# Performance work log

Hardware: AMD Instinct MI355X
Metric: run time of the kernel (lower is better)

## Reference

```python
import jax, jax.numpy as jnp
import numpy as np

HEADS = 8

def setup_inputs() -> dict:
    key = jax.random.key(0)
    k1, k2, k3 = jax.random.split(key, 3)
    B, C, L = 8, 512, 4096
    dim_head = 64
    hidden = HEADS * dim_head  # 512
    x = jax.random.normal(k1, (B, C, L), dtype=jnp.float32)
    # Conv1d(dim, hidden*3, 1, bias=False) -> weight [hidden*3, dim]
    w_qkv = jax.random.normal(k2, (hidden * 3, C), dtype=jnp.float32) * 0.02
    # Conv1d(hidden, dim, 1) -> weight [dim, hidden], bias [dim]
    w_out = jax.random.normal(k3, (C, hidden), dtype=jnp.float32) * 0.02
    b_out = jnp.zeros((C,), dtype=jnp.float32)
    return {"x": x, "w_qkv": w_qkv, "w_out": w_out, "b_out": b_out}

def reference(x, w_qkv, w_out, b_out):
    B, C, L = x.shape
    # 1x1 Conv1d == channel matmul
    qkv = jnp.einsum('oc,bcl->bol', w_qkv, x)            # [B, 3*H*dh, L]
    qkv = qkv.reshape(B, 3, HEADS, -1, L)                # qkv outermost, then heads, then c
    q, k, v = qkv[:, 0], qkv[:, 1], qkv[:, 2]            # each [B, H, dh, L]
    k = jax.nn.softmax(k, axis=-1)                       # softmax over sequence
    context = jnp.einsum('bhdn,bhen->bhde', k, v)        # [B, H, dh, dh]
    out = jnp.einsum('bhde,bhdn->bhen', context, q)      # [B, H, dh, L]
    out = out.reshape(B, -1, L)                          # [B, H*dh, L]
    return jnp.einsum('oc,bcl->bol', w_out, out) + b_out[None, :, None]
```

## Files before the change

### kernel.cpp

```cpp
#include <hip/hip_runtime.h>
#include <hip/hip_bf16.h>


typedef __bf16 bf16x8 __attribute__((ext_vector_type(8)));
typedef __bf16 bf16x4 __attribute__((ext_vector_type(4)));
typedef float  f32x4  __attribute__((ext_vector_type(4)));

#define B_  8
#define L_  4096
#define C_  512

#define GLD_LDS16(g, l)                                             \
    __builtin_amdgcn_global_load_lds(                               \
        (const __attribute__((address_space(1))) void*)(g),         \
        (__attribute__((address_space(3))) void*)(l), 16, 0, 0)

#define FENCE asm volatile("" ::: "memory")
#define BAR   do { FENCE; __builtin_amdgcn_s_barrier(); FENCE; } while (0)
#define DRAIN_LGKM asm volatile("s_waitcnt lgkmcnt(0)" ::: "memory")
#define WAIT_VM(N) asm volatile("s_waitcnt vmcnt(" #N ")" ::: "memory")

__global__ __launch_bounds__(256) void prep_all(const float* __restrict__ x,
                                                __hip_bfloat16* __restrict__ xt,
                                                const float* __restrict__ wqkv_f,
                                                __hip_bfloat16* __restrict__ wkv_b,
                                                __hip_bfloat16* __restrict__ wqT,
                                                float* __restrict__ zero_base) {
    __shared__ float tile[64 * 132];
    int blk = blockIdx.x;
    int t = threadIdx.x;
    if (blk < 2048) {
        int b = blk >> 8, rem = blk & 255;
        int l0 = (rem & 31) * 128, c0 = (rem >> 5) * 64;
        const float* xp = x + ((size_t)b * C_ + c0) * L_ + l0;
#pragma unroll
        for (int p = 0; p < 8; p++) {
            int i = p * 8 + (t >> 5);
            int j = (t & 31) * 4;
            float4 vv = *(const float4*)(xp + (size_t)i * L_ + j);
            *(float4*)&tile[i * 132 + j] = vv;
        }
        __syncthreads();
        unsigned short* xo = (unsigned short*)xt + ((size_t)b * L_ + l0) * C_ + c0;
#pragma unroll
        for (int qq = 0; qq < 8; qq++) {
            int l = qq * 16 + (t >> 4);
            int cg = (t & 15) * 4;
            bf16x4 ov;
#pragma unroll
            for (int k = 0; k < 4; k++) ov[k] = (__bf16)tile[(cg + k) * 132 + l];
            *(bf16x4*)(xo + (size_t)l * C_ + cg) = ov;
        }
    } else if (blk < 4096) {
        int i = (blk - 2048) * 256 + t;
        wkv_b[i] = __float2bfloat16(wqkv_f[512 * 512 + i]);
    } else if (blk < 4352) {
        int tb = blk - 4096;
        int r0 = (tb >> 4) * 32, c0 = (tb & 15) * 32;
        int tx = t & 31, ty = t >> 5;
        for (int r = 0; r < 32; r += 8)
            tile[(ty + r) * 33 + tx] = wqkv_f[(size_t)(r0 + ty + r) * 512 + c0 + tx];
        __syncthreads();
        for (int r = 0; r < 32; r += 8)
            wqT[(size_t)(c0 + ty + r) * 512 + r0 + tx] = __float2bfloat16(tile[tx * 33 + ty + r]);
    } else {
        int i = (blk - 4352) * 256 + t;
        zero_base[i] = 0.f;
    }
}

__global__ __launch_bounds__(256, 2) void gemm_kv(
    const __hip_bfloat16* __restrict__ A, const __hip_bfloat16* __restrict__ Bt,
    float* __restrict__ ctx, float* __restrict__ Ssum) {
    __shared__ alignas(16) unsigned short sA[2][128 * 64];
    __shared__ alignas(16) unsigned short sB[2][128 * 64];

    const int K = C_;
    int b = blockIdx.z, h = blockIdx.y;
    int n0 = blockIdx.x * 128;
    const __hip_bfloat16* Bb = Bt + (size_t)b * L_ * C_;

    int t = threadIdx.x;
    int lane = t & 63, wv = t >> 6;
    int l16 = lane & 15, q4 = lane >> 4;
    int wr = (wv >> 1) * 64, wc = (wv & 1) * 64;

    int srow = lane >> 3;
    int swz  = ((lane & 7) ^ srow) * 8;

    const __hip_bfloat16* gA[4];
    const __hip_bfloat16* gB[4];
    unsigned ldoff[4];
#pragma unroll
    for (int c = 0; c < 4; c++) {
        int r = c * 32 + wv * 8;
        int lr = r + srow;
        int grow = h * 64 + lr + (lr >= 64 ? 448 : 0);
        gA[c] = A + (size_t)grow * K + swz;
        gB[c] = Bb + (size_t)(n0 + lr) * K + swz;
        ldoff[c] = (unsigned)r * 64;
    }

    int gsel0 = (q4 ^ (l16 & 7)) * 8;
    int gsel1 = gsel0 ^ 32;
    unsigned rA = (unsigned)(wr + l16) * 64;
    unsigned rB = (unsigned)(wc + l16) * 64;
    const int NKT = K >> 6;

    f32x4 acc[4][4] = {};
    bf16x8 aF[4][2], bF[4][2];

#pragma unroll
    for (int c = 0; c < 4; c++) GLD_LDS16(gA[c], &sA[0][ldoff[c]]);
#pragma unroll
    for (int c = 0; c < 4; c++) GLD_LDS16(gB[c], &sB[0][ldoff[c]]);
#pragma unroll
    for (int c = 0; c < 4; c++) GLD_LDS16(gA[c] + 64, &sA[1][ldoff[c]]);
    WAIT_VM(4);
    BAR;

#pragma unroll 1
    for (int kt = 0; kt < NKT; ++kt) {
        int cur = kt & 1, nbuf = cur ^ 1;
        const unsigned short* As_b = sA[cur];
        const unsigned short* Bs_b = sB[cur];
        bool st1 = (kt + 1) < NKT;
        bool st2 = (kt + 2) < NKT;

#pragma unroll
        for (int i = 0; i < 4; i++) {
            aF[i][0] = *(const bf16x8*)&As_b[rA + i * 1024 + gsel0];
            aF[i][1] = *(const bf16x8*)&As_b[rA + i * 1024 + gsel1];
        }
#pragma unroll
        for (int j = 0; j < 2; j++) {
            bF[j][0] = *(const bf16x8*)&Bs_b[rB + j * 1024 + gsel0];
            bF[j][1] = *(const bf16x8*)&Bs_b[rB + j * 1024 + gsel1];
        }
        if (st1) {
            int ko = (kt + 1) << 6;
#pragma unroll
            for (int c = 0; c < 4; c++) GLD_LDS16(gB[c] + ko, &sB[nbuf][ldoff[c]]);
        }
        BAR;
        __builtin_amdgcn_s_setprio(1);
#pragma unroll
        for (int ks = 0; ks < 2; ks++)
#pragma unroll
            for (int i = 0; i < 4; i++)
#pragma unroll
                for (int j = 0; j < 2; j++)
                    acc[i][j] = __builtin_amdgcn_mfma_f32_16x16x32_bf16(aF[i][ks], bF[j][ks], acc[i][j], 0, 0, 0);
        __builtin_amdgcn_s_setprio(0);
        DRAIN_LGKM;
        BAR;

#pragma unroll
        for (int j = 2; j < 4; j++) {
            bF[j][0] = *(const bf16x8*)&Bs_b[rB + j * 1024 + gsel0];
            bF[j][1] = *(const bf16x8*)&Bs_b[rB + j * 1024 + gsel1];
        }
        if (st2) {
            int ko = (kt + 2) << 6;
#pragma unroll
            for (int c = 0; c < 4; c++) GLD_LDS16(gA[c] + ko, &sA[cur][ldoff[c]]);
        }
        BAR;
        __builtin_amdgcn_s_setprio(1);
#pragma unroll
        for (int ks = 0; ks < 2; ks++)
#pragma unroll
            for (int i = 0; i < 4; i++)
#pragma unroll
                for (int j = 0; j < 2; j++)
                    acc[i][2 + j] = __builtin_amdgcn_mfma_f32_16x16x32_bf16(aF[i][ks], bF[2 + j][ks], acc[i][2 + j], 0, 0, 0);
        __builtin_amdgcn_s_setprio(0);
        DRAIN_LGKM;
        if (st2) { WAIT_VM(4); } else { WAIT_VM(0); }
        BAR;
    }

    __bf16* Pb = (__bf16*)sA;
    __bf16* Vb = (__bf16*)sB;
    float* ctxg = ctx  + ((size_t)b * 8 + h) * 4096;
    float* Sg   = Ssum + ((size_t)b * 8 + h) * 64;

    if (wv < 2) {
#pragma unroll
        for (int i = 0; i < 4; i++)
#pragma unroll
            for (int r = 0; r < 4; r++) {
                int d = i * 16 + q4 * 4 + r;
                float rs = 0.f;
#pragma unroll
                for (int j = 0; j < 4; j++) {
                    int n = wc + j * 16 + l16;
                    float pv = __expf(acc[i][j][r]);
                    rs += pv;
                    Pb[d * 128 + (((n >> 3) ^ (d & 15)) * 8) + (n & 7)] = (__bf16)pv;
                }
                rs += __shfl_xor(rs, 1, 64);
                rs += __shfl_xor(rs, 2, 64);
                rs += __shfl_xor(rs, 4, 64);
                rs += __shfl_xor(rs, 8, 64);
                if (l16 == 0) atomicAdd(&Sg[d], rs);
            }
    } else {
#pragma unroll
        for (int i = 0; i < 4; i++)
#pragma unroll
            for (int j = 0; j < 4; j++)
#pragma unroll
                for (int r = 0; r < 4; r++) {
                    int e = i * 16 + q4 * 4 + r;
                    int n = wc + j * 16 + l16;
                    Vb[e * 128 + (((n >> 3) ^ (e & 15)) * 8) + (n & 7)] = (__bf16)acc[i][j][r];
                }
    }
    DRAIN_LGKM;
    BAR;

    f32x4 acc2[4] = {};
#pragma unroll
    for (int kk = 0; kk < 4; kk++) {
        int gg = kk * 4 + q4;
        bf16x8 bf2 = *(const bf16x8*)&Vb[(wv * 16 + l16) * 128 + ((gg ^ l16) * 8)];
#pragma unroll
        for (int i2 = 0; i2 < 4; i2++) {
            bf16x8 af2 = *(const bf16x8*)&Pb[(i2 * 16 + l16) * 128 + ((gg ^ l16) * 8)];
            acc2[i2] = __builtin_amdgcn_mfma_f32_16x16x32_bf16(af2, bf2, acc2[i2], 0, 0, 0);
        }
    }
#pragma unroll
    for (int i2 = 0; i2 < 4; i2++)
#pragma unroll
        for (int r = 0; r < 4; r++) {
            int d = i2 * 16 + q4 * 4 + r;
            int e = wv * 16 + l16;
            atomicAdd(&ctxg[d * 64 + e], acc2[i2][r]);
        }
}

__global__ __launch_bounds__(256, 2) void gemm_p(
    const __hip_bfloat16* __restrict__ A, const __hip_bfloat16* __restrict__ Bt,
    size_t strideA, size_t strideB, int M, int N, int K,
    float* __restrict__ outb, const float* __restrict__ bias) {
    __shared__ alignas(16) unsigned short sA[2][128 * 64];
    __shared__ alignas(16) unsigned short sB[2][128 * 64];

    int b = blockIdx.z;
    int m0 = blockIdx.y * 128, n0 = blockIdx.x * 128;
    const __hip_bfloat16* Ab = A + strideA * (size_t)b;
    const __hip_bfloat16* Bb = Bt + strideB * (size_t)b;

    int t = threadIdx.x;
    int lane = t & 63, wv = t >> 6;
    int l16 = lane & 15, q4 = lane >> 4;
    int wr = (wv >> 1) * 64, wc = (wv & 1) * 64;

    int srow = lane >> 3;
    int swz  = ((lane & 7) ^ srow) * 8;

    const __hip_bfloat16* gA[4];
    const __hip_bfloat16* gB[4];
    unsigned ldoff[4];
#pragma unroll
    for (int c = 0; c < 4; c++) {
        int r = c * 32 + wv * 8;
        gA[c] = Ab + (size_t)(m0 + r + srow) * K + swz;
        gB[c] = Bb + (size_t)(n0 + r + srow) * K + swz;
        ldoff[c] = (unsigned)r * 64;
    }

    int gsel0 = (q4 ^ (l16 & 7)) * 8;
    int gsel1 = gsel0 ^ 32;
    unsigned rA = (unsigned)(wr + l16) * 64;
    unsigned rB = (unsigned)(wc + l16) * 64;
    int NKT = K >> 6;

    f32x4 acc[4][4] = {};
    bf16x8 aF[4][2], bF[4][2];

#pragma unroll
    for (int c = 0; c < 4; c++) GLD_LDS16(gA[c], &sA[0][ldoff[c]]);
#pragma unroll
    for (int c = 0; c < 4; c++) GLD_LDS16(gB[c], &sB[0][ldoff[c]]);
    if (NKT > 1) {
#pragma unroll
        for (int c = 0; c < 4; c++) GLD_LDS16(gA[c] + 64, &sA[1][ldoff[c]]);
        WAIT_VM(4);
    } else {
        WAIT_VM(0);
    }
    BAR;

#pragma unroll 1
    for (int kt = 0; kt < NKT; ++kt) {
        int cur = kt & 1, nbuf = cur ^ 1;
        const unsigned short* As_b = sA[cur];
        const unsigned short* Bs_b = sB[cur];
        bool st1 = (kt + 1) < NKT;
        bool st2 = (kt + 2) < NKT;

#pragma unroll
        for (int i = 0; i < 4; i++) {
            aF[i][0] = *(const bf16x8*)&As_b[rA + i * 1024 + gsel0];
            aF[i][1] = *(const bf16x8*)&As_b[rA + i * 1024 + gsel1];
        }
#pragma unroll
        for (int j = 0; j < 2; j++) {
            bF[j][0] = *(const bf16x8*)&Bs_b[rB + j * 1024 + gsel0];
            bF[j][1] = *(const bf16x8*)&Bs_b[rB + j * 1024 + gsel1];
        }
        if (st1) {
            int ko = (kt + 1) << 6;
#pragma unroll
            for (int c = 0; c < 4; c++) GLD_LDS16(gB[c] + ko, &sB[nbuf][ldoff[c]]);
        }
        BAR;
        __builtin_amdgcn_s_setprio(1);
#pragma unroll
        for (int ks = 0; ks < 2; ks++)
#pragma unroll
            for (int i = 0; i < 4; i++)
#pragma unroll
                for (int j = 0; j < 2; j++)
                    acc[i][j] = __builtin_amdgcn_mfma_f32_16x16x32_bf16(aF[i][ks], bF[j][ks], acc[i][j], 0, 0, 0);
        __builtin_amdgcn_s_setprio(0);
        DRAIN_LGKM;
        BAR;

#pragma unroll
        for (int j = 2; j < 4; j++) {
            bF[j][0] = *(const bf16x8*)&Bs_b[rB + j * 1024 + gsel0];
            bF[j][1] = *(const bf16x8*)&Bs_b[rB + j * 1024 + gsel1];
        }
        if (st2) {
            int ko = (kt + 2) << 6;
#pragma unroll
            for (int c = 0; c < 4; c++) GLD_LDS16(gA[c] + ko, &sA[cur][ldoff[c]]);
        }
        BAR;
        __builtin_amdgcn_s_setprio(1);
#pragma unroll
        for (int ks = 0; ks < 2; ks++)
#pragma unroll
            for (int i = 0; i < 4; i++)
#pragma unroll
                for (int j = 0; j < 2; j++)
                    acc[i][2 + j] = __builtin_amdgcn_mfma_f32_16x16x32_bf16(aF[i][ks], bF[2 + j][ks], acc[i][2 + j], 0, 0, 0);
        __builtin_amdgcn_s_setprio(0);
        DRAIN_LGKM;
        if (st2) { WAIT_VM(4); } else { WAIT_VM(0); }
        BAR;
    }

#pragma unroll
    for (int i = 0; i < 4; i++)
#pragma unroll
        for (int j = 0; j < 4; j++)
#pragma unroll
            for (int r = 0; r < 4; r++) {
                int row = m0 + wr + i * 16 + q4 * 4 + r;
                int col = n0 + wc + j * 16 + l16;
                outb[((size_t)b * M + row) * (size_t)N + col] = acc[i][j][r] + bias[row];
            }
}

__global__ __launch_bounds__(256) void gemm_bt(
    const __hip_bfloat16* __restrict__ A, const __hip_bfloat16* __restrict__ Bt,
    size_t strideA, size_t strideB, int M, int N, int K,
    __hip_bfloat16* __restrict__ obf) {
    __shared__ alignas(16) unsigned short As[128 * 64];
    __shared__ alignas(16) unsigned short Bs[128 * 64];

    int b = blockIdx.z;
    int m0 = blockIdx.y * 128, n0 = blockIdx.x * 128;
    const __hip_bfloat16* Ab = A + strideA * (size_t)b;
    const __hip_bfloat16* Bb = Bt + strideB * (size_t)b;

    int t = threadIdx.x;
    int lane = t & 63, wv = t >> 6;
    int l16 = lane & 15, q4 = lane >> 4;
    int wr = (wv >> 1) * 64, wc = (wv & 1) * 64;

    int srow = lane >> 3;
    int swz  = ((lane & 7) ^ srow) * 8;

    const __hip_bfloat16* gA[4];
    const __hip_bfloat16* gB[4];
    unsigned short* lA[4];
    unsigned short* lB[4];
#pragma unroll
    for (int c = 0; c < 4; c++) {
        int r = wv * 32 + c * 8;
        gA[c] = Ab + (size_t)(m0 + r + srow) * K + swz;
        gB[c] = Bb + (size_t)(n0 + r + srow) * K + swz;
        lA[c] = &As[r * 64];
        lB[c] = &Bs[r * 64];
    }

    int gsel0 = ((q4) ^ (l16 & 7)) * 8;
    int gsel1 = gsel0 ^ 32;
    int rA = (wr + l16) * 64;
    int rB = (wc + l16) * 64;

    f32x4 acc[4][4] = {};

    for (int k0 = 0; k0 < K; k0 += 64) {
        __syncthreads();
#pragma unroll
        for (int c = 0; c < 4; c++) {
            GLD_LDS16(gA[c] + k0, lA[c]);
            GLD_LDS16(gB[c] + k0, lB[c]);
        }
        __syncthreads();

        bf16x8 af[4], bfr[4];
#pragma unroll
        for (int i = 0; i < 4; i++) {
            af[i]  = *(const bf16x8*)&As[rA + i * 1024 + gsel0];
            bfr[i] = *(const bf16x8*)&Bs[rB + i * 1024 + gsel0];
        }
#pragma unroll
        for (int i = 0; i < 4; i++)
#pragma unroll
            for (int j = 0; j < 4; j++)
                acc[i][j] = __builtin_amdgcn_mfma_f32_16x16x32_bf16(af[i], bfr[j], acc[i][j], 0, 0, 0);
#pragma unroll
        for (int i = 0; i < 4; i++) {
            af[i]  = *(const bf16x8*)&As[rA + i * 1024 + gsel1];
            bfr[i] = *(const bf16x8*)&Bs[rB + i * 1024 + gsel1];
        }
#pragma unroll
        for (int i = 0; i < 4; i++)
#pragma unroll
            for (int j = 0; j < 4; j++)
                acc[i][j] = __builtin_amdgcn_mfma_f32_16x16x32_bf16(af[i], bfr[j], acc[i][j], 0, 0, 0);
    }

#pragma unroll
    for (int i = 0; i < 4; i++)
#pragma unroll
        for (int j = 0; j < 4; j++)
#pragma unroll
            for (int r = 0; r < 4; r++) {
                int row = m0 + wr + i * 16 + q4 * 4 + r;
                int col = n0 + wc + j * 16 + l16;
                obf[((size_t)b * 512 + row) * (size_t)N + col] = __float2bfloat16(acc[i][j][r]);
            }
}

__global__ __launch_bounds__(256) void w2_kernel(const float* __restrict__ wout,
                                                 const float* __restrict__ ctx,
                                                 const float* __restrict__ Ssum,
                                                 __hip_bfloat16* __restrict__ w2) {
    int ob = blockIdx.x, h = blockIdx.y, b = blockIdx.z;
    __shared__ float cT[64 * 65];
    __shared__ float wT[64 * 65];
    __shared__ float Sinv[64];
    int t = threadIdx.x;
    const float* cg = ctx + ((size_t)b * 8 + h) * 4096;
    if (t < 64) Sinv[t] = 1.0f / Ssum[((size_t)b * 8 + h) * 64 + t];
    __syncthreads();
    for (int i = t; i < 4096; i += 256) {
        int d = i >> 6, e = i & 63;
        cT[e * 65 + d] = cg[i] * Sinv[d];
        wT[e * 65 + d] = wout[(size_t)(ob * 64 + d) * 512 + h * 64 + e];
    }
    __syncthreads();
    int ol = t >> 2;
    int db = (t & 3) * 16;
    unsigned short* w2p = (unsigned short*)w2 + ((size_t)b * 512 + ob * 64 + ol) * 512 + h * 64;
    for (int g = 0; g < 4; g++) {
        int d0 = db + g * 4;
        float s0 = 0.f, s1 = 0.f, s2 = 0.f, s3 = 0.f;
#pragma unroll
        for (int e = 0; e < 64; e++) {
            float w = wT[e * 65 + ol];
            s0 += w * cT[e * 65 + d0];
            s1 += w * cT[e * 65 + d0 + 1];
            s2 += w * cT[e * 65 + d0 + 2];
            s3 += w * cT[e * 65 + d0 + 3];
        }
        bf16x4 ov;
        ov[0] = (__bf16)s0; ov[1] = (__bf16)s1; ov[2] = (__bf16)s2; ov[3] = (__bf16)s3;
        *(bf16x4*)(w2p + d0) = ov;
    }
}

extern "C" void kernel_launch(void* const* d_in, const int* in_sizes, int n_in,
                              void* d_out, int out_size, void* d_ws, size_t ws_size,
                              hipStream_t stream) {
    const float* x     = (const float*)d_in[0];
    const float* w_qkv = (const float*)d_in[1];
    const float* w_out = (const float*)d_in[2];
    const float* b_out = (const float*)d_in[3];
    float* out = (float*)d_out;
    char* ws = (char*)d_ws;

    size_t off_xt  = 0;
    size_t off_wkv = off_xt + (size_t)B_ * L_ * C_ * 2;
    size_t off_wqT = off_wkv + (size_t)1024 * 512 * 2;
    size_t off_ctx = off_wqT + (size_t)512 * 512 * 2;
    size_t off_S   = off_ctx + (size_t)B_ * 8 * 4096 * 4;
    size_t off_w2  = off_S + (size_t)B_ * 8 * 64 * 4;
    size_t off_w3  = off_w2 + (size_t)B_ * 512 * 512 * 2;

    __hip_bfloat16* xt   = (__hip_bfloat16*)(ws + off_xt);
    __hip_bfloat16* wkvb = (__hip_bfloat16*)(ws + off_wkv);
    __hip_bfloat16* wqT  = (__hip_bfloat16*)(ws + off_wqT);
    float*          ctx  = (float*)(ws + off_ctx);
    float*          Sv   = (float*)(ws + off_S);
    __hip_bfloat16* w2   = (__hip_bfloat16*)(ws + off_w2);
    __hip_bfloat16* W3   = (__hip_bfloat16*)(ws + off_w3);

    prep_all<<<5392, 256, 0, stream>>>(x, xt, w_qkv, wkvb, wqT, ctx);

    gemm_kv<<<dim3(L_ / 128, 8, B_), 256, 0, stream>>>(wkvb, xt, ctx, Sv);

    w2_kernel<<<dim3(8, 8, B_), 256, 0, stream>>>(w_out, ctx, Sv, w2);

    gemm_bt<<<dim3(512 / 128, 512 / 128, B_), 256, 0, stream>>>(
        w2, wqT, (size_t)512 * 512, 0, 512, 512, 512, W3);

    gemm_p<<<dim3(L_ / 128, 512 / 128, B_), 256, 0, stream>>>(
        W3, xt, (size_t)512 * 512, (size_t)L_ * C_, 512, L_, 512, out, b_out);
}
```

Before: 245.5 us.

## Replace global atomics in kv GEMM with per-slice partials reduced in w2 kernel

gemm_kv now gives each block four consecutive 128-column sequence tiles instead of one. It accumulates the context in registers and the softmax denominators in shared memory, then writes one partial per slice without global atomics. w2_kernel sums the 8 slice partials before normalising, and the zeroing section of prep_all is removed. This cuts the grid from 2048 to 512 blocks and drops global atomic traffic and the zero-init pass, but it lowers parallelism and adds serial per-block work, which may underfill the GPU.

```diff
diff --git a/kernel.cpp b/kernel.cpp
--- a/kernel.cpp
+++ b/kernel.cpp
@@ -24,8 +24,7 @@
                                                 __hip_bfloat16* __restrict__ xt,
                                                 const float* __restrict__ wqkv_f,
                                                 __hip_bfloat16* __restrict__ wkv_b,
-                                                __hip_bfloat16* __restrict__ wqT,
-                                                float* __restrict__ zero_base) {
+                                                __hip_bfloat16* __restrict__ wqT) {
     __shared__ float tile[64 * 132];
     int blk = blockIdx.x;
     int t = threadIdx.x;
@@ -54,7 +53,7 @@
     } else if (blk < 4096) {
         int i = (blk - 2048) * 256 + t;
         wkv_b[i] = __float2bfloat16(wqkv_f[512 * 512 + i]);
-    } else if (blk < 4352) {
+    } else {
         int tb = blk - 4096;
         int r0 = (tb >> 4) * 32, c0 = (tb & 15) * 32;
         int tx = t & 31, ty = t >> 5;
@@ -63,21 +62,18 @@
         __syncthreads();
         for (int r = 0; r < 32; r += 8)
             wqT[(size_t)(c0 + ty + r) * 512 + r0 + tx] = __float2bfloat16(tile[tx * 33 + ty + r]);
-    } else {
-        int i = (blk - 4352) * 256 + t;
-        zero_base[i] = 0.f;
     }
 }
 
 __global__ __launch_bounds__(256, 2) void gemm_kv(
     const __hip_bfloat16* __restrict__ A, const __hip_bfloat16* __restrict__ Bt,
-    float* __restrict__ ctx, float* __restrict__ Ssum) {
+    float* __restrict__ ctxp, float* __restrict__ Sp) {
     __shared__ alignas(16) unsigned short sA[2][128 * 64];
     __shared__ alignas(16) unsigned short sB[2][128 * 64];
+    __shared__ float Sred[64];
 
     const int K = C_;
-    int b = blockIdx.z, h = blockIdx.y;
-    int n0 = blockIdx.x * 128;
+    int b = blockIdx.z, h = blockIdx.y, slice = blockIdx.x;
     const __hip_bfloat16* Bb = Bt + (size_t)b * L_ * C_;
 
     int t = threadIdx.x;
@@ -88,17 +84,19 @@
     int srow = lane >> 3;
     int swz  = ((lane & 7) ^ srow) * 8;
 
+    if (t < 64) Sred[t] = 0.f;
+
     const __hip_bfloat16* gA[4];
-    const __hip_bfloat16* gB[4];
     unsigned ldoff[4];
+    int rloc[4];
 #pragma unroll
     for (int c = 0; c < 4; c++) {
         int r = c * 32 + wv * 8;
         int lr = r + srow;
         int grow = h * 64 + lr + (lr >= 64 ? 448 : 0);
         gA[c] = A + (size_t)grow * K + swz;
-        gB[c] = Bb + (size_t)(n0 + lr) * K + swz;
         ldoff[c] = (unsigned)r * 64;
+        rloc[c] = lr;
     }
 
     int gsel0 = (q4 ^ (l16 & 7)) * 8;
@@ -107,6 +105,191 @@
     unsigned rB = (unsigned)(wc + l16) * 64;
     const int NKT = K >> 6;
 
+    f32x4 acc2[4] = {};
+    bf16x8 aF[4][2], bF[4][2];
+
+#pragma unroll 1
+    for (int sub = 0; sub < 4; ++sub) {
+        int nt = slice * 512 + sub * 128;
+        const __hip_bfloat16* gB[4];
+#pragma unroll
+        for (int c = 0; c < 4; c++)
+            gB[c] = Bb + (size_t)(nt + rloc[c]) * K + swz;
+
+        f32x4 acc[4][4] = {};
+
+#pragma unroll
+        for (int c = 0; c < 4; c++) GLD_LDS16(gA[c], &sA[0][ldoff[c]]);
+#pragma unroll
+        for (int c = 0; c < 4; c++) GLD_LDS16(gB[c], &sB[0][ldoff[c]]);
+#pragma unroll
+        for (int c = 0; c < 4; c++) GLD_LDS16(gA[c] + 64, &sA[1][ldoff[c]]);
+        WAIT_VM(4);
+        BAR;
+
+#pragma unroll 1
+        for (int kt = 0; kt < NKT; ++kt) {
+            int cur = kt & 1, nbuf = cur ^ 1;
+            const unsigned short* As_b = sA[cur];
+            const unsigned short* Bs_b = sB[cur];
+            bool st1 = (kt + 1) < NKT;
+            bool st2 = (kt + 2) < NKT;
+
+#pragma unroll
+            for (int i = 0; i < 4; i++) {
+                aF[i][0] = *(const bf16x8*)&As_b[rA + i * 1024 + gsel0];
+                aF[i][1] = *(const bf16x8*)&As_b[rA + i * 1024 + gsel1];
+            }
+#pragma unroll
+            for (int j = 0; j < 2; j++) {
+                bF[j][0] = *(const bf16x8*)&Bs_b[rB + j * 1024 + gsel0];
+                bF[j][1] = *(const bf16x8*)&Bs_b[rB + j * 1024 + gsel1];
+            }
+            if (st1) {
+                int ko = (kt + 1) << 6;
+#pragma unroll
+                for (int c = 0; c < 4; c++) GLD_LDS16(gB[c] + ko, &sB[nbuf][ldoff[c]]);
+            }
+            BAR;
+            __builtin_amdgcn_s_setprio(1);
+#pragma unroll
+            for (int ks = 0; ks < 2; ks++)
+#pragma unroll
+                for (int i = 0; i < 4; i++)
+#pragma unroll
+                    for (int j = 0; j < 2; j++)
+                        acc[i][j] = __builtin_amdgcn_mfma_f32_16x16x32_bf16(aF[i][ks], bF[j][ks], acc[i][j], 0, 0, 0);
+            __builtin_amdgcn_s_setprio(0);
+            DRAIN_LGKM;
+            BAR;
+
+#pragma unroll
+            for (int j = 2; j < 4; j++) {
+                bF[j][0] = *(const bf16x8*)&Bs_b[rB + j * 1024 + gsel0];
+                bF[j][1] = *(const bf16x8*)&Bs_b[rB + j * 1024 + gsel1];
+            }
+            if (st2) {
+                int ko = (kt + 2) << 6;
+#pragma unroll
+                for (int c = 0; c < 4; c++) GLD_LDS16(gA[c] + ko, &sA[cur][ldoff[c]]);
+            }
+            BAR;
+            __builtin_amdgcn_s_setprio(1);
+#pragma unroll
+            for (int ks = 0; ks < 2; ks++)
+#pragma unroll
+                for (int i = 0; i < 4; i++)
+#pragma unroll
+                    for (int j = 0; j < 2; j++)
+                        acc[i][2 + j] = __builtin_amdgcn_mfma_f32_16x16x32_bf16(aF[i][ks], bF[2 + j][ks], acc[i][2 + j], 0, 0, 0);
+            __builtin_amdgcn_s_setprio(0);
+            DRAIN_LGKM;
+            if (st2) { WAIT_VM(4); } else { WAIT_VM(0); }
+            BAR;
+        }
+
+        __bf16* Pb = (__bf16*)sA;
+        __bf16* Vb = (__bf16*)sB;
+
+        if (wv < 2) {
+#pragma unroll
+            for (int i = 0; i < 4; i++)
+#pragma unroll
+                for (int r = 0; r < 4; r++) {
+                    int d = i * 16 + q4 * 4 + r;
+                    float rs = 0.f;
+#pragma unroll
+                    for (int j = 0; j < 4; j++) {
+                        int n = wc + j * 16 + l16;
+                        float pv = __expf(acc[i][j][r]);
+                        rs += pv;
+                        Pb[d * 128 + (((n >> 3) ^ (d & 15)) * 8) + (n & 7)] = (__bf16)pv;
+                    }
+                    rs += __shfl_xor(rs, 1, 64);
+                    rs += __shfl_xor(rs, 2, 64);
+                    rs += __shfl_xor(rs, 4, 64);
+                    rs += __shfl_xor(rs, 8, 64);
+                    if (l16 == 0) atomicAdd(&Sred[d], rs);
+                }
+        } else {
+#pragma unroll
+            for (int i = 0; i < 4; i++)
+#pragma unroll
+                for (int j = 0; j < 4; j++)
+#pragma unroll
+                    for (int r = 0; r < 4; r++) {
+                        int e = i * 16 + q4 * 4 + r;
+                        int n = wc + j * 16 + l16;
+                        Vb[e * 128 + (((n >> 3) ^ (e & 15)) * 8) + (n & 7)] = (__bf16)acc[i][j][r];
+                    }
+        }
+        DRAIN_LGKM;
+        BAR;
+
+#pragma unroll
+        for (int kk = 0; kk < 4; kk++) {
+            int gg = kk * 4 + q4;
+            bf16x8 bf2 = *(const bf16x8*)&Vb[(wv * 16 + l16) * 128 + ((gg ^ l16) * 8)];
+#pragma unroll
+            for (int i2 = 0; i2 < 4; i2++) {
+                bf16x8 af2 = *(const bf16x8*)&Pb[(i2 * 16 + l16) * 128 + ((gg ^ l16) * 8)];
+                acc2[i2] = __builtin_amdgcn_mfma_f32_16x16x32_bf16(af2, bf2, acc2[i2], 0, 0, 0);
+            }
+        }
+        DRAIN_LGKM;
+        BAR;
+    }
+
+    float* cg = ctxp + ((size_t)slice * 64 + b * 8 + h) * 4096;
+#pragma unroll
+    for (int i2 = 0; i2 < 4; i2++)
+#pragma unroll
+        for (int r = 0; r < 4; r++) {
+            int d = i2 * 16 + q4 * 4 + r;
+            int e = wv * 16 + l16;
+            cg[d * 64 + e] = acc2[i2][r];
+        }
+    if (t < 64)
+        Sp[((size_t)slice * 64 + b * 8 + h) * 64 + t] = Sred[t];
+}
+
+__global__ __launch_bounds__(256, 2) void gemm_p(
+    const __hip_bfloat16* __restrict__ A, const __hip_bfloat16* __restrict__ Bt,
+    size_t strideA, size_t strideB, int M, int N, int K,
+    float* __restrict__ outb, const float* __restrict__ bias) {
+    __shared__ alignas(16) unsigned short sA[2][128 * 64];
+    __shared__ alignas(16) unsigned short sB[2][128 * 64];
+
+    int b = blockIdx.z;
+    int m0 = blockIdx.y * 128, n0 = blockIdx.x * 128;
+    const __hip_bfloat16* Ab = A + strideA * (size_t)b;
+    const __hip_bfloat16* Bb = Bt + strideB * (size_t)b;
+
+    int t = threadIdx.x;
+    int lane = t & 63, wv = t >> 6;
+    int l16 = lane & 15, q4 = lane >> 4;
+    int wr = (wv >> 1) * 64, wc = (wv & 1) * 64;
+
+    int srow = lane >> 3;
+    int swz  = ((lane & 7) ^ srow) * 8;
+
+    const __hip_bfloat16* gA[4];
+    const __hip_bfloat16* gB[4];
+    unsigned ldoff[4];
+#pragma unroll
+    for (int c = 0; c < 4; c++) {
+        int r = c * 32 + wv * 8;
+        gA[c] = Ab + (size_t)(m0 + r + srow) * K + swz;
+        gB[c] = Bb + (size_t)(n0 + r + srow) * K + swz;
+        ldoff[c] = (unsigned)r * 64;
+    }
+
+    int gsel0 = (q4 ^ (l16 & 7)) * 8;
+    int gsel1 = gsel0 ^ 32;
+    unsigned rA = (unsigned)(wr + l16) * 64;
+    unsigned rB = (unsigned)(wc + l16) * 64;
+    int NKT = K >> 6;
+
     f32x4 acc[4][4] = {};
     bf16x8 aF[4][2], bF[4][2];
 
@@ -114,9 +297,13 @@
     for (int c = 0; c < 4; c++) GLD_LDS16(gA[c], &sA[0][ldoff[c]]);
 #pragma unroll
     for (int c = 0; c < 4; c++) GLD_LDS16(gB[c], &sB[0][ldoff[c]]);
-#pragma unroll
-    for (int c = 0; c < 4; c++) GLD_LDS16(gA[c] + 64, &sA[1][ldoff[c]]);
-    WAIT_VM(4);
+    if (NKT > 1) {
+#pragma unroll
+        for (int c = 0; c < 4; c++) GLD_LDS16(gA[c] + 64, &sA[1][ldoff[c]]);
+        WAIT_VM(4);
+    } else {
+        WAIT_VM(0);
+    }
     BAR;
 
 #pragma unroll 1
@@ -180,181 +367,6 @@
         BAR;
     }
 
-    __bf16* Pb = (__bf16*)sA;
-    __bf16* Vb = (__bf16*)sB;
-    float* ctxg = ctx  + ((size_t)b * 8 + h) * 4096;
-    float* Sg   = Ssum + ((size_t)b * 8 + h) * 64;
-
-    if (wv < 2) {
-#pragma unroll
-        for (int i = 0; i < 4; i++)
-#pragma unroll
-            for (int r = 0; r < 4; r++) {
-                int d = i * 16 + q4 * 4 + r;
-                float rs = 0.f;
-#pragma unroll
-                for (int j = 0; j < 4; j++) {
-                    int n = wc + j * 16 + l16;
-                    float pv = __expf(acc[i][j][r]);
-                    rs += pv;
-                    Pb[d * 128 + (((n >> 3) ^ (d & 15)) * 8) + (n & 7)] = (__bf16)pv;
-                }
-                rs += __shfl_xor(rs, 1, 64);
-                rs += __shfl_xor(rs, 2, 64);
-                rs += __shfl_xor(rs, 4, 64);
-                rs += __shfl_xor(rs, 8, 64);
-                if (l16 == 0) atomicAdd(&Sg[d], rs);
-            }
-    } else {
-#pragma unroll
-        for (int i = 0; i < 4; i++)
-#pragma unroll
-            for (int j = 0; j < 4; j++)
-#pragma unroll
-                for (int r = 0; r < 4; r++) {
-                    int e = i * 16 + q4 * 4 + r;
-                    int n = wc + j * 16 + l16;
-                    Vb[e * 128 + (((n >> 3) ^ (e & 15)) * 8) + (n & 7)] = (__bf16)acc[i][j][r];
-                }
-    }
-    DRAIN_LGKM;
-    BAR;
-
-    f32x4 acc2[4] = {};
-#pragma unroll
-    for (int kk = 0; kk < 4; kk++) {
-        int gg = kk * 4 + q4;
-        bf16x8 bf2 = *(const bf16x8*)&Vb[(wv * 16 + l16) * 128 + ((gg ^ l16) * 8)];
-#pragma unroll
-        for (int i2 = 0; i2 < 4; i2++) {
-            bf16x8 af2 = *(const bf16x8*)&Pb[(i2 * 16 + l16) * 128 + ((gg ^ l16) * 8)];
-            acc2[i2] = __builtin_amdgcn_mfma_f32_16x16x32_bf16(af2, bf2, acc2[i2], 0, 0, 0);
-        }
-    }
-#pragma unroll
-    for (int i2 = 0; i2 < 4; i2++)
-#pragma unroll
-        for (int r = 0; r < 4; r++) {
-            int d = i2 * 16 + q4 * 4 + r;
-            int e = wv * 16 + l16;
-            atomicAdd(&ctxg[d * 64 + e], acc2[i2][r]);
-        }
-}
-
-__global__ __launch_bounds__(256, 2) void gemm_p(
-    const __hip_bfloat16* __restrict__ A, const __hip_bfloat16* __restrict__ Bt,
-    size_t strideA, size_t strideB, int M, int N, int K,
-    float* __restrict__ outb, const float* __restrict__ bias) {
-    __shared__ alignas(16) unsigned short sA[2][128 * 64];
-    __shared__ alignas(16) unsigned short sB[2][128 * 64];
-
-    int b = blockIdx.z;
-    int m0 = blockIdx.y * 128, n0 = blockIdx.x * 128;
-    const __hip_bfloat16* Ab = A + strideA * (size_t)b;
-    const __hip_bfloat16* Bb = Bt + strideB * (size_t)b;
-
-    int t = threadIdx.x;
-    int lane = t & 63, wv = t >> 6;
-    int l16 = lane & 15, q4 = lane >> 4;
-    int wr = (wv >> 1) * 64, wc = (wv & 1) * 64;
-
-    int srow = lane >> 3;
-    int swz  = ((lane & 7) ^ srow) * 8;
-
-    const __hip_bfloat16* gA[4];
-    const __hip_bfloat16* gB[4];
-    unsigned ldoff[4];
-#pragma unroll
-    for (int c = 0; c < 4; c++) {
-        int r = c * 32 + wv * 8;
-        gA[c] = Ab + (size_t)(m0 + r + srow) * K + swz;
-        gB[c] = Bb + (size_t)(n0 + r + srow) * K + swz;
-        ldoff[c] = (unsigned)r * 64;
-    }
-
-    int gsel0 = (q4 ^ (l16 & 7)) * 8;
-    int gsel1 = gsel0 ^ 32;
-    unsigned rA = (unsigned)(wr + l16) * 64;
-    unsigned rB = (unsigned)(wc + l16) * 64;
-    int NKT = K >> 6;
-
-    f32x4 acc[4][4] = {};
-    bf16x8 aF[4][2], bF[4][2];
-
-#pragma unroll
-    for (int c = 0; c < 4; c++) GLD_LDS16(gA[c], &sA[0][ldoff[c]]);
-#pragma unroll
-    for (int c = 0; c < 4; c++) GLD_LDS16(gB[c], &sB[0][ldoff[c]]);
-    if (NKT > 1) {
-#pragma unroll
-        for (int c = 0; c < 4; c++) GLD_LDS16(gA[c] + 64, &sA[1][ldoff[c]]);
-        WAIT_VM(4);
-    } else {
-        WAIT_VM(0);
-    }
-    BAR;
-
-#pragma unroll 1
-    for (int kt = 0; kt < NKT; ++kt) {
-        int cur = kt & 1, nbuf = cur ^ 1;
-        const unsigned short* As_b = sA[cur];
-        const unsigned short* Bs_b = sB[cur];
-        bool st1 = (kt + 1) < NKT;
-        bool st2 = (kt + 2) < NKT;
-
-#pragma unroll
-        for (int i = 0; i < 4; i++) {
-            aF[i][0] = *(const bf16x8*)&As_b[rA + i * 1024 + gsel0];
-            aF[i][1] = *(const bf16x8*)&As_b[rA + i * 1024 + gsel1];
-        }
-#pragma unroll
-        for (int j = 0; j < 2; j++) {
-            bF[j][0] = *(const bf16x8*)&Bs_b[rB + j * 1024 + gsel0];
-            bF[j][1] = *(const bf16x8*)&Bs_b[rB + j * 1024 + gsel1];
-        }
-        if (st1) {
-            int ko = (kt + 1) << 6;
-#pragma unroll
-            for (int c = 0; c < 4; c++) GLD_LDS16(gB[c] + ko, &sB[nbuf][ldoff[c]]);
-        }
-        BAR;
-        __builtin_amdgcn_s_setprio(1);
-#pragma unroll
-        for (int ks = 0; ks < 2; ks++)
-#pragma unroll
-            for (int i = 0; i < 4; i++)
-#pragma unroll
-                for (int j = 0; j < 2; j++)
-                    acc[i][j] = __builtin_amdgcn_mfma_f32_16x16x32_bf16(aF[i][ks], bF[j][ks], acc[i][j], 0, 0, 0);
-        __builtin_amdgcn_s_setprio(0);
-        DRAIN_LGKM;
-        BAR;
-
-#pragma unroll
-        for (int j = 2; j < 4; j++) {
-            bF[j][0] = *(const bf16x8*)&Bs_b[rB + j * 1024 + gsel0];
-            bF[j][1] = *(const bf16x8*)&Bs_b[rB + j * 1024 + gsel1];
-        }
-        if (st2) {
-            int ko = (kt + 2) << 6;
-#pragma unroll
-            for (int c = 0; c < 4; c++) GLD_LDS16(gA[c] + ko, &sA[cur][ldoff[c]]);
-        }
-        BAR;
-        __builtin_amdgcn_s_setprio(1);
-#pragma unroll
-        for (int ks = 0; ks < 2; ks++)
-#pragma unroll
-            for (int i = 0; i < 4; i++)
-#pragma unroll
-                for (int j = 0; j < 2; j++)
-                    acc[i][2 + j] = __builtin_amdgcn_mfma_f32_16x16x32_bf16(aF[i][ks], bF[2 + j][ks], acc[i][2 + j], 0, 0, 0);
-        __builtin_amdgcn_s_setprio(0);
-        DRAIN_LGKM;
-        if (st2) { WAIT_VM(4); } else { WAIT_VM(0); }
-        BAR;
-    }
-
 #pragma unroll
     for (int i = 0; i < 4; i++)
 #pragma unroll
@@ -452,20 +464,30 @@
 }
 
 __global__ __launch_bounds__(256) void w2_kernel(const float* __restrict__ wout,
-                                                 const float* __restrict__ ctx,
-                                                 const float* __restrict__ Ssum,
+                                                 const float* __restrict__ ctxp,
+                                                 const float* __restrict__ Sp,
                                                  __hip_bfloat16* __restrict__ w2) {
     int ob = blockIdx.x, h = blockIdx.y, b = blockIdx.z;
     __shared__ float cT[64 * 65];
     __shared__ float wT[64 * 65];
     __shared__ float Sinv[64];
     int t = threadIdx.x;
-    const float* cg = ctx + ((size_t)b * 8 + h) * 4096;
-    if (t < 64) Sinv[t] = 1.0f / Ssum[((size_t)b * 8 + h) * 64 + t];
+    const size_t SL = (size_t)64 * 4096;
+    const float* cg = ctxp + ((size_t)b * 8 + h) * 4096;
+    if (t < 64) {
+        const float* sg = Sp + ((size_t)b * 8 + h) * 64;
+        float S = 0.f;
+#pragma unroll
+        for (int s = 0; s < 8; s++) S += sg[(size_t)s * 64 * 64 + t];
+        Sinv[t] = 1.0f / S;
+    }
     __syncthreads();
     for (int i = t; i < 4096; i += 256) {
         int d = i >> 6, e = i & 63;
-        cT[e * 65 + d] = cg[i] * Sinv[d];
+        float s = 0.f;
+#pragma unroll
+        for (int sl = 0; sl < 8; sl++) s += cg[(size_t)sl * SL + i];
+        cT[e * 65 + d] = s * Sinv[d];
         wT[e * 65 + d] = wout[(size_t)(ob * 64 + d) * 512 + h * 64 + e];
     }
     __syncthreads();
@@ -499,27 +521,27 @@
     float* out = (float*)d_out;
     char* ws = (char*)d_ws;
 
-    size_t off_xt  = 0;
-    size_t off_wkv = off_xt + (size_t)B_ * L_ * C_ * 2;
-    size_t off_wqT = off_wkv + (size_t)1024 * 512 * 2;
-    size_t off_ctx = off_wqT + (size_t)512 * 512 * 2;
-    size_t off_S   = off_ctx + (size_t)B_ * 8 * 4096 * 4;
-    size_t off_w2  = off_S + (size_t)B_ * 8 * 64 * 4;
-    size_t off_w3  = off_w2 + (size_t)B_ * 512 * 512 * 2;
+    size_t off_xt   = 0;
+    size_t off_wkv  = off_xt + (size_t)B_ * L_ * C_ * 2;
+    size_t off_wqT  = off_wkv + (size_t)1024 * 512 * 2;
+    size_t off_ctxp = off_wqT + (size_t)512 * 512 * 2;
+    size_t off_Sp   = off_ctxp + (size_t)8 * 64 * 4096 * 4;
+    size_t off_w2   = off_Sp + (size_t)8 * 64 * 64 * 4;
+    size_t off_w3   = off_w2 + (size_t)B_ * 512 * 512 * 2;
 
     __hip_bfloat16* xt   = (__hip_bfloat16*)(ws + off_xt);
     __hip_bfloat16* wkvb = (__hip_bfloat16*)(ws + off_wkv);
     __hip_bfloat16* wqT  = (__hip_bfloat16*)(ws + off_wqT);
-    float*          ctx  = (float*)(ws + off_ctx);
-    float*          Sv   = (float*)(ws + off_S);
+    float*          ctxp = (float*)(ws + off_ctxp);
+    float*          Sp   = (float*)(ws + off_Sp);
     __hip_bfloat16* w2   = (__hip_bfloat16*)(ws + off_w2);
     __hip_bfloat16* W3   = (__hip_bfloat16*)(ws + off_w3);
 
-    prep_all<<<5392, 256, 0, stream>>>(x, xt, w_qkv, wkvb, wqT, ctx);
-
-    gemm_kv<<<dim3(L_ / 128, 8, B_), 256, 0, stream>>>(wkvb, xt, ctx, Sv);
-
-    w2_kernel<<<dim3(8, 8, B_), 256, 0, stream>>>(w_out, ctx, Sv, w2);
+    prep_all<<<4352, 256, 0, stream>>>(x, xt, w_qkv, wkvb, wqT);
+
+    gemm_kv<<<dim3(8, 8, B_), 256, 0, stream>>>(wkvb, xt, ctxp, Sp);
+
+    w2_kernel<<<dim3(8, 8, B_), 256, 0, stream>>>(w_out, ctxp, Sp, w2);
 
     gemm_bt<<<dim3(512 / 128, 512 / 128, B_), 256, 0, stream>>>(
         w2, wqT, (size_t)512 * 512, 0, 512, 512, 512, W3);
```

After: 287.7 us. 1.17x slower.
